# Kernel tuning notes

Hardware: AMD Instinct MI355X
Metric: run time of the kernel (lower is better)

Reference implementation:

```python
import jax, jax.numpy as jnp
import numpy as np

T, J, D = 65536, 512, 128

def setup_inputs() -> dict:
    key = jax.random.key(0)
    k1, k2 = jax.random.split(key)
    u = jax.random.normal(k1, (1, J, D), dtype=jnp.float32)
    s = jax.random.normal(k2, (T, J), dtype=jnp.float32)
    return {"u": u, "s": s}

def reference(u, s):
    # softmax over the query axis (axis=1 of s, matching tf softmax(s, axis=1))
    A = jax.nn.softmax(s, axis=1)          # [T, J]
    # sum_j A[t, j] * u[0, j, :]  == A @ u[0]
    c2q = jnp.einsum('tj,jd->td', A, u[0])  # [T, D]
    return c2q.T                            # [D, T], matching tf.transpose(c2q)
```

## Files before the change

### kernel.cpp

```cpp
#include <hip/hip_runtime.h>
#include <hip/hip_bf16.h>


constexpr int T_DIM = 65536;
constexpr int J_DIM = 512;
constexpr int D_DIM = 128;
constexpr int KK_STEPS = J_DIM / 32;
constexpr int NFRAG = 8;
constexpr int PF_DEPTH = 4;
constexpr int BP_ELEMS = KK_STEPS * NFRAG * 64;

typedef __attribute__((ext_vector_type(4))) float  f32x4;
typedef __attribute__((ext_vector_type(8))) short  s16x8;
typedef __attribute__((ext_vector_type(8))) __bf16 bf16x8;

__device__ __forceinline__ short f2bf_rne(float f) {
    unsigned u = __builtin_bit_cast(unsigned, f);
    u += 0x7fffu + ((u >> 16) & 1u);
    return (short)(u >> 16);
}

__global__ __launch_bounds__(512, 2) void c2q_main(const float* __restrict__ sm,
                                                   const float* __restrict__ u,
                                                   float* __restrict__ out) {
    __shared__ s16x8 bsh[BP_ELEMS];

    const int tid  = threadIdx.x;
    const int l    = tid & 63;
    const int w    = tid >> 6;
    const int lmod = l & 15;
    const int lh   = l >> 4;
    const int r0   = blockIdx.x * 128 + w * 16;

    const float* sp = sm + (size_t)(r0 + lmod) * J_DIM + lh * 8;

    f32x4 sbuf[PF_DEPTH][2];
#pragma unroll
    for (int p = 0; p < PF_DEPTH; ++p) {
        sbuf[p][0] = *reinterpret_cast<const f32x4*>(sp + p * 32);
        sbuf[p][1] = *reinterpret_cast<const f32x4*>(sp + p * 32 + 4);
    }

#pragma unroll 4
    for (int it = 0; it < BP_ELEMS / 512; ++it) {
        int e  = it * 512 + tid;
        int d  = ((e >> 6) & (NFRAG - 1)) * 16 + (e & 15);
        int k0 = (e >> 9) * 32 + 8 * ((e >> 4) & 3);
        const float* up = u + (size_t)k0 * D_DIM + d;
        s16x8 o;
#pragma unroll
        for (int i = 0; i < 8; ++i)
            o[i] = f2bf_rne(up[(size_t)i * D_DIM]);
        bsh[e] = o;
    }
    __syncthreads();

    f32x4 acc[NFRAG];
#pragma unroll
    for (int nf = 0; nf < NFRAG; ++nf) acc[nf] = (f32x4){0.f, 0.f, 0.f, 0.f};
    float den = 0.f;

#pragma unroll
    for (int kk = 0; kk < KK_STEPS; ++kk) {
        f32x4 s0 = sbuf[kk & (PF_DEPTH - 1)][0];
        f32x4 s1 = sbuf[kk & (PF_DEPTH - 1)][1];
        if (kk + PF_DEPTH < KK_STEPS) {
            sbuf[kk & (PF_DEPTH - 1)][0] =
                *reinterpret_cast<const f32x4*>(sp + (kk + PF_DEPTH) * 32);
            sbuf[kk & (PF_DEPTH - 1)][1] =
                *reinterpret_cast<const f32x4*>(sp + (kk + PF_DEPTH) * 32 + 4);
        }
        float e0 = __expf(s0[0]), e1 = __expf(s0[1]);
        float e2 = __expf(s0[2]), e3 = __expf(s0[3]);
        float e4 = __expf(s1[0]), e5 = __expf(s1[1]);
        float e6 = __expf(s1[2]), e7 = __expf(s1[3]);
        den += ((e0 + e1) + (e2 + e3)) + ((e4 + e5) + (e6 + e7));
        s16x8 a;
        a[0] = f2bf_rne(e0); a[1] = f2bf_rne(e1);
        a[2] = f2bf_rne(e2); a[3] = f2bf_rne(e3);
        a[4] = f2bf_rne(e4); a[5] = f2bf_rne(e5);
        a[6] = f2bf_rne(e6); a[7] = f2bf_rne(e7);
        bf16x8 av = __builtin_bit_cast(bf16x8, a);
#pragma unroll
        for (int nf = 0; nf < NFRAG; ++nf) {
            bf16x8 bv = __builtin_bit_cast(bf16x8, bsh[(kk * NFRAG + nf) * 64 + l]);
            acc[nf] = __builtin_amdgcn_mfma_f32_16x16x32_bf16(av, bv, acc[nf], 0, 0, 0);
        }
        __builtin_amdgcn_sched_barrier(0);
    }

    den += __shfl_xor(den, 16, 64);
    den += __shfl_xor(den, 32, 64);
    float inv[4];
#pragma unroll
    for (int r = 0; r < 4; ++r)
        inv[r] = 1.0f / __shfl(den, 4 * lh + r, 64);

#pragma unroll
    for (int nf = 0; nf < NFRAG; ++nf) {
        f32x4 v;
#pragma unroll
        for (int r = 0; r < 4; ++r) v[r] = acc[nf][r] * inv[r];
        *reinterpret_cast<f32x4*>(out + (size_t)(nf * 16 + lmod) * T_DIM
                                  + r0 + 4 * lh) = v;
    }
}

extern "C" void kernel_launch(void* const* d_in, const int* in_sizes, int n_in,
                              void* d_out, int out_size, void* d_ws, size_t ws_size,
                              hipStream_t stream) {
    const float* u = (const float*)d_in[0];
    const float* s = (const float*)d_in[1];
    float* out = (float*)d_out;

    c2q_main<<<T_DIM / 128, 512, 0, stream>>>(s, u, out);
}
```

Before: 38.72 us.

## Process two row tiles per block to amortize LDS B-fragment staging

Each block now handles 256 rows in two passes of 128, reusing the bf16 u fragments staged in shared memory and halving the number of blocks that convert u. The s prefetch ring is deepened to 6 and continues across the pass boundary, so loads for the second tile are issued while the first is still computing. This adds register pressure from the deeper prefetch and halves the grid to 256 blocks, which may leave fewer waves to hide latency.

Result: faster. 36.75 us (-5.1%).

```diff
diff --git a/kernel.cpp b/kernel.cpp
--- a/kernel.cpp
+++ b/kernel.cpp
@@ -7,7 +7,7 @@
 constexpr int D_DIM = 128;
 constexpr int KK_STEPS = J_DIM / 32;
 constexpr int NFRAG = 8;
-constexpr int PF_DEPTH = 4;
+constexpr int PF_DEPTH = 6;
 constexpr int BP_ELEMS = KK_STEPS * NFRAG * 64;
 
 typedef __attribute__((ext_vector_type(4))) float  f32x4;
@@ -30,15 +30,16 @@
     const int w    = tid >> 6;
     const int lmod = l & 15;
     const int lh   = l >> 4;
-    const int r0   = blockIdx.x * 128 + w * 16;
+    const int r0   = blockIdx.x * 256 + w * 16;
 
-    const float* sp = sm + (size_t)(r0 + lmod) * J_DIM + lh * 8;
+    const float* sp0 = sm + (size_t)(r0 + lmod) * J_DIM + lh * 8;
+    const float* sp1 = sp0 + 128 * J_DIM;
 
     f32x4 sbuf[PF_DEPTH][2];
 #pragma unroll
     for (int p = 0; p < PF_DEPTH; ++p) {
-        sbuf[p][0] = *reinterpret_cast<const f32x4*>(sp + p * 32);
-        sbuf[p][1] = *reinterpret_cast<const f32x4*>(sp + p * 32 + 4);
+        sbuf[p][0] = *reinterpret_cast<const f32x4*>(sp0 + p * 32);
+        sbuf[p][1] = *reinterpret_cast<const f32x4*>(sp0 + p * 32 + 4);
     }
 
 #pragma unroll 4
@@ -55,54 +56,62 @@
     }
     __syncthreads();
 
-    f32x4 acc[NFRAG];
 #pragma unroll
-    for (int nf = 0; nf < NFRAG; ++nf) acc[nf] = (f32x4){0.f, 0.f, 0.f, 0.f};
-    float den = 0.f;
+    for (int p = 0; p < 2; ++p) {
+        const int rp = r0 + p * 128;
+
+        f32x4 acc[NFRAG];
+#pragma unroll
+        for (int nf = 0; nf < NFRAG; ++nf) acc[nf] = (f32x4){0.f, 0.f, 0.f, 0.f};
+        float den = 0.f;
 
 #pragma unroll
-    for (int kk = 0; kk < KK_STEPS; ++kk) {
-        f32x4 s0 = sbuf[kk & (PF_DEPTH - 1)][0];
-        f32x4 s1 = sbuf[kk & (PF_DEPTH - 1)][1];
-        if (kk + PF_DEPTH < KK_STEPS) {
-            sbuf[kk & (PF_DEPTH - 1)][0] =
-                *reinterpret_cast<const f32x4*>(sp + (kk + PF_DEPTH) * 32);
-            sbuf[kk & (PF_DEPTH - 1)][1] =
-                *reinterpret_cast<const f32x4*>(sp + (kk + PF_DEPTH) * 32 + 4);
+        for (int kk = 0; kk < KK_STEPS; ++kk) {
+            const int g    = p * KK_STEPS + kk;
+            const int slot = g % PF_DEPTH;
+            f32x4 s0 = sbuf[slot][0];
+            f32x4 s1 = sbuf[slot][1];
+            if (g + PF_DEPTH < 2 * KK_STEPS) {
+                const int   f  = g + PF_DEPTH;
+                const float* b = (f < KK_STEPS) ? sp0 : sp1;
+                const int   tk = f & (KK_STEPS - 1);
+                sbuf[slot][0] = *reinterpret_cast<const f32x4*>(b + tk * 32);
+                sbuf[slot][1] = *reinterpret_cast<const f32x4*>(b + tk * 32 + 4);
+            }
+            float e0 = __expf(s0[0]), e1 = __expf(s0[1]);
+            float e2 = __expf(s0[2]), e3 = __expf(s0[3]);
+            float e4 = __expf(s1[0]), e5 = __expf(s1[1]);
+            float e6 = __expf(s1[2]), e7 = __expf(s1[3]);
+            den += ((e0 + e1) + (e2 + e3)) + ((e4 + e5) + (e6 + e7));
+            s16x8 a;
+            a[0] = f2bf_rne(e0); a[1] = f2bf_rne(e1);
+            a[2] = f2bf_rne(e2); a[3] = f2bf_rne(e3);
+            a[4] = f2bf_rne(e4); a[5] = f2bf_rne(e5);
+            a[6] = f2bf_rne(e6); a[7] = f2bf_rne(e7);
+            bf16x8 av = __builtin_bit_cast(bf16x8, a);
+#pragma unroll
+            for (int nf = 0; nf < NFRAG; ++nf) {
+                bf16x8 bv = __builtin_bit_cast(bf16x8, bsh[(kk * NFRAG + nf) * 64 + l]);
+                acc[nf] = __builtin_amdgcn_mfma_f32_16x16x32_bf16(av, bv, acc[nf], 0, 0, 0);
+            }
+            __builtin_amdgcn_sched_barrier(0);
         }
-        float e0 = __expf(s0[0]), e1 = __expf(s0[1]);
-        float e2 = __expf(s0[2]), e3 = __expf(s0[3]);
-        float e4 = __expf(s1[0]), e5 = __expf(s1[1]);
-        float e6 = __expf(s1[2]), e7 = __expf(s1[3]);
-        den += ((e0 + e1) + (e2 + e3)) + ((e4 + e5) + (e6 + e7));
-        s16x8 a;
-        a[0] = f2bf_rne(e0); a[1] = f2bf_rne(e1);
-        a[2] = f2bf_rne(e2); a[3] = f2bf_rne(e3);
-        a[4] = f2bf_rne(e4); a[5] = f2bf_rne(e5);
-        a[6] = f2bf_rne(e6); a[7] = f2bf_rne(e7);
-        bf16x8 av = __builtin_bit_cast(bf16x8, a);
+
+        den += __shfl_xor(den, 16, 64);
+        den += __shfl_xor(den, 32, 64);
+        float inv[4];
+#pragma unroll
+        for (int r = 0; r < 4; ++r)
+            inv[r] = 1.0f / __shfl(den, 4 * lh + r, 64);
+
 #pragma unroll
         for (int nf = 0; nf < NFRAG; ++nf) {
-            bf16x8 bv = __builtin_bit_cast(bf16x8, bsh[(kk * NFRAG + nf) * 64 + l]);
-            acc[nf] = __builtin_amdgcn_mfma_f32_16x16x32_bf16(av, bv, acc[nf], 0, 0, 0);
+            f32x4 v;
+#pragma unroll
+            for (int r = 0; r < 4; ++r) v[r] = acc[nf][r] * inv[r];
+            *reinterpret_cast<f32x4*>(out + (size_t)(nf * 16 + lmod) * T_DIM
+                                      + rp + 4 * lh) = v;
         }
-        __builtin_amdgcn_sched_barrier(0);
-    }
-
-    den += __shfl_xor(den, 16, 64);
-    den += __shfl_xor(den, 32, 64);
-    float inv[4];
-#pragma unroll
-    for (int r = 0; r < 4; ++r)
-        inv[r] = 1.0f / __shfl(den, 4 * lh + r, 64);
-
-#pragma unroll
-    for (int nf = 0; nf < NFRAG; ++nf) {
-        f32x4 v;
-#pragma unroll
-        for (int r = 0; r < 4; ++r) v[r] = acc[nf][r] * inv[r];
-        *reinterpret_cast<f32x4*>(out + (size_t)(nf * 16 + lmod) * T_DIM
-                                  + r0 + 4 * lh) = v;
     }
 }
 
@@ -113,5 +122,5 @@
     const float* s = (const float*)d_in[1];
     float* out = (float*)d_out;
 
-    c2q_main<<<T_DIM / 128, 512, 0, stream>>>(s, u, out);
+    c2q_main<<<T_DIM / 256, 512, 0, stream>>>(s, u, out);
 }
```

## Split bf16 B staging into two half-size LDS passes to cut shared memory

Applied to the files above, without the earlier changes.

The converted u operand is now staged in LDS in two halves (first 256 rows, then the remaining 256) instead of all 512 rows at once, which halves the shared-memory footprint per block. The likely aim is to fit more blocks per CU, or ease LDS pressure, so more s-row streaming is in flight. In exchange it adds two block-wide barriers and a second fill partway through the K loop, which stalls all waves while the second half is converted from global memory.

After: 42.28 us. 9.2% more time.

```diff
diff --git a/kernel.cpp b/kernel.cpp
--- a/kernel.cpp
+++ b/kernel.cpp
@@ -5,10 +5,11 @@
 constexpr int T_DIM = 65536;
 constexpr int J_DIM = 512;
 constexpr int D_DIM = 128;
-constexpr int KK_STEPS = J_DIM / 32;
+constexpr int KK_PER_PASS = 8;
+constexpr int NSTEP = 16;
 constexpr int NFRAG = 8;
 constexpr int PF_DEPTH = 4;
-constexpr int BP_ELEMS = KK_STEPS * NFRAG * 64;
+constexpr int BP_ELEMS = KK_PER_PASS * NFRAG * 64;
 
 typedef __attribute__((ext_vector_type(4))) float  f32x4;
 typedef __attribute__((ext_vector_type(8))) short  s16x8;
@@ -18,6 +19,22 @@
     unsigned u = __builtin_bit_cast(unsigned, f);
     u += 0x7fffu + ((u >> 16) & 1u);
     return (short)(u >> 16);
+}
+
+__device__ __forceinline__ void fill_b(int pass, const float* __restrict__ u,
+                                       s16x8* __restrict__ bsh, int tid) {
+#pragma unroll 4
+    for (int it = 0; it < BP_ELEMS / 512; ++it) {
+        int e  = it * 512 + tid;
+        int d  = ((e >> 6) & (NFRAG - 1)) * 16 + (e & 15);
+        int k0 = pass * 256 + (e >> 9) * 32 + 8 * ((e >> 4) & 3);
+        const float* up = u + (size_t)k0 * D_DIM + d;
+        s16x8 o;
+#pragma unroll
+        for (int i = 0; i < 8; ++i)
+            o[i] = f2bf_rne(up[(size_t)i * D_DIM]);
+        bsh[e] = o;
+    }
 }
 
 __global__ __launch_bounds__(512, 2) void c2q_main(const float* __restrict__ sm,
@@ -41,18 +58,7 @@
         sbuf[p][1] = *reinterpret_cast<const f32x4*>(sp + p * 32 + 4);
     }
 
-#pragma unroll 4
-    for (int it = 0; it < BP_ELEMS / 512; ++it) {
-        int e  = it * 512 + tid;
-        int d  = ((e >> 6) & (NFRAG - 1)) * 16 + (e & 15);
-        int k0 = (e >> 9) * 32 + 8 * ((e >> 4) & 3);
-        const float* up = u + (size_t)k0 * D_DIM + d;
-        s16x8 o;
-#pragma unroll
-        for (int i = 0; i < 8; ++i)
-            o[i] = f2bf_rne(up[(size_t)i * D_DIM]);
-        bsh[e] = o;
-    }
+    fill_b(0, u, bsh, tid);
     __syncthreads();
 
     f32x4 acc[NFRAG];
@@ -61,14 +67,20 @@
     float den = 0.f;
 
 #pragma unroll
-    for (int kk = 0; kk < KK_STEPS; ++kk) {
-        f32x4 s0 = sbuf[kk & (PF_DEPTH - 1)][0];
-        f32x4 s1 = sbuf[kk & (PF_DEPTH - 1)][1];
-        if (kk + PF_DEPTH < KK_STEPS) {
-            sbuf[kk & (PF_DEPTH - 1)][0] =
-                *reinterpret_cast<const f32x4*>(sp + (kk + PF_DEPTH) * 32);
-            sbuf[kk & (PF_DEPTH - 1)][1] =
-                *reinterpret_cast<const f32x4*>(sp + (kk + PF_DEPTH) * 32 + 4);
+    for (int g = 0; g < NSTEP; ++g) {
+        if (g == KK_PER_PASS) {
+            __syncthreads();
+            fill_b(1, u, bsh, tid);
+            __syncthreads();
+        }
+        const int slot = g & (PF_DEPTH - 1);
+        f32x4 s0 = sbuf[slot][0];
+        f32x4 s1 = sbuf[slot][1];
+        if (g + PF_DEPTH < NSTEP) {
+            sbuf[slot][0] =
+                *reinterpret_cast<const f32x4*>(sp + (g + PF_DEPTH) * 32);
+            sbuf[slot][1] =
+                *reinterpret_cast<const f32x4*>(sp + (g + PF_DEPTH) * 32 + 4);
         }
         float e0 = __expf(s0[0]), e1 = __expf(s0[1]);
         float e2 = __expf(s0[2]), e3 = __expf(s0[3]);
@@ -81,6 +93,7 @@
         a[4] = f2bf_rne(e4); a[5] = f2bf_rne(e5);
         a[6] = f2bf_rne(e6); a[7] = f2bf_rne(e7);
         bf16x8 av = __builtin_bit_cast(bf16x8, a);
+        const int kk = g & (KK_PER_PASS - 1);
 #pragma unroll
         for (int nf = 0; nf < NFRAG; ++nf) {
             bf16x8 bv = __builtin_bit_cast(bf16x8, bsh[(kk * NFRAG + nf) * 64 + l]);
```

## Switch to 32x32x16 MFMA tiles with 32 rows per wave

Applied to the files above, without the earlier changes.

Replaces the 16x16x32 bf16 MFMA with 32x32x16, so each wave handles 32 rows of s and each block handles 256. Each iteration loads and exponentiates twice as many s values per lane, and the B operand layout in LDS is repacked to match. This aims to cut LDS reads and MFMA instruction overhead per output. The cost is that the grid shrinks to half as many blocks, which lowers parallelism across CUs, and the accumulators use more registers.

New measurement: 51.14 us. +32.1%, slower.

```diff
diff --git a/kernel.cpp b/kernel.cpp
--- a/kernel.cpp
+++ b/kernel.cpp
@@ -5,14 +5,15 @@
 constexpr int T_DIM = 65536;
 constexpr int J_DIM = 512;
 constexpr int D_DIM = 128;
-constexpr int KK_STEPS = J_DIM / 32;
-constexpr int NFRAG = 8;
+constexpr int KK = 16;
+constexpr int NFRAG = 4;
 constexpr int PF_DEPTH = 4;
-constexpr int BP_ELEMS = KK_STEPS * NFRAG * 64;
+constexpr int BP_ELEMS = KK * 2 * NFRAG * 64;
 
-typedef __attribute__((ext_vector_type(4))) float  f32x4;
-typedef __attribute__((ext_vector_type(8))) short  s16x8;
-typedef __attribute__((ext_vector_type(8))) __bf16 bf16x8;
+typedef __attribute__((ext_vector_type(4)))  float  f32x4;
+typedef __attribute__((ext_vector_type(16))) float  f32x16;
+typedef __attribute__((ext_vector_type(8)))  short  s16x8;
+typedef __attribute__((ext_vector_type(8)))  __bf16 bf16x8;
 
 __device__ __forceinline__ short f2bf_rne(float f) {
     unsigned u = __builtin_bit_cast(unsigned, f);
@@ -28,24 +29,26 @@
     const int tid  = threadIdx.x;
     const int l    = tid & 63;
     const int w    = tid >> 6;
-    const int lmod = l & 15;
-    const int lh   = l >> 4;
-    const int r0   = blockIdx.x * 128 + w * 16;
+    const int l31  = l & 31;
+    const int lh5  = l >> 5;
+    const int r0w  = blockIdx.x * 256 + w * 32;
 
-    const float* sp = sm + (size_t)(r0 + lmod) * J_DIM + lh * 8;
+    const float* sp = sm + (size_t)(r0w + l31) * J_DIM + lh5 * 8;
 
-    f32x4 sbuf[PF_DEPTH][2];
+    f32x4 sbuf[PF_DEPTH][4];
 #pragma unroll
     for (int p = 0; p < PF_DEPTH; ++p) {
         sbuf[p][0] = *reinterpret_cast<const f32x4*>(sp + p * 32);
         sbuf[p][1] = *reinterpret_cast<const f32x4*>(sp + p * 32 + 4);
+        sbuf[p][2] = *reinterpret_cast<const f32x4*>(sp + p * 32 + 16);
+        sbuf[p][3] = *reinterpret_cast<const f32x4*>(sp + p * 32 + 20);
     }
 
 #pragma unroll 4
     for (int it = 0; it < BP_ELEMS / 512; ++it) {
         int e  = it * 512 + tid;
-        int d  = ((e >> 6) & (NFRAG - 1)) * 16 + (e & 15);
-        int k0 = (e >> 9) * 32 + 8 * ((e >> 4) & 3);
+        int d  = ((e >> 6) & 3) * 32 + (e & 31);
+        int k0 = (e >> 9) * 32 + ((e >> 8) & 1) * 16 + ((e >> 5) & 1) * 8;
         const float* up = u + (size_t)k0 * D_DIM + d;
         s16x8 o;
 #pragma unroll
@@ -55,54 +58,80 @@
     }
     __syncthreads();
 
-    f32x4 acc[NFRAG];
+    f32x16 acc[NFRAG];
 #pragma unroll
-    for (int nf = 0; nf < NFRAG; ++nf) acc[nf] = (f32x4){0.f, 0.f, 0.f, 0.f};
+    for (int nf = 0; nf < NFRAG; ++nf)
+#pragma unroll
+        for (int r = 0; r < 16; ++r) acc[nf][r] = 0.f;
     float den = 0.f;
 
 #pragma unroll
-    for (int kk = 0; kk < KK_STEPS; ++kk) {
-        f32x4 s0 = sbuf[kk & (PF_DEPTH - 1)][0];
-        f32x4 s1 = sbuf[kk & (PF_DEPTH - 1)][1];
-        if (kk + PF_DEPTH < KK_STEPS) {
-            sbuf[kk & (PF_DEPTH - 1)][0] =
-                *reinterpret_cast<const f32x4*>(sp + (kk + PF_DEPTH) * 32);
-            sbuf[kk & (PF_DEPTH - 1)][1] =
-                *reinterpret_cast<const f32x4*>(sp + (kk + PF_DEPTH) * 32 + 4);
+    for (int g = 0; g < KK; ++g) {
+        const int slot = g & (PF_DEPTH - 1);
+        f32x4 s0 = sbuf[slot][0];
+        f32x4 s1 = sbuf[slot][1];
+        f32x4 s2 = sbuf[slot][2];
+        f32x4 s3 = sbuf[slot][3];
+        if (g + PF_DEPTH < KK) {
+            const float* b = sp + (g + PF_DEPTH) * 32;
+            sbuf[slot][0] = *reinterpret_cast<const f32x4*>(b);
+            sbuf[slot][1] = *reinterpret_cast<const f32x4*>(b + 4);
+            sbuf[slot][2] = *reinterpret_cast<const f32x4*>(b + 16);
+            sbuf[slot][3] = *reinterpret_cast<const f32x4*>(b + 20);
         }
         float e0 = __expf(s0[0]), e1 = __expf(s0[1]);
         float e2 = __expf(s0[2]), e3 = __expf(s0[3]);
         float e4 = __expf(s1[0]), e5 = __expf(s1[1]);
         float e6 = __expf(s1[2]), e7 = __expf(s1[3]);
-        den += ((e0 + e1) + (e2 + e3)) + ((e4 + e5) + (e6 + e7));
-        s16x8 a;
-        a[0] = f2bf_rne(e0); a[1] = f2bf_rne(e1);
-        a[2] = f2bf_rne(e2); a[3] = f2bf_rne(e3);
-        a[4] = f2bf_rne(e4); a[5] = f2bf_rne(e5);
-        a[6] = f2bf_rne(e6); a[7] = f2bf_rne(e7);
-        bf16x8 av = __builtin_bit_cast(bf16x8, a);
+        float f0 = __expf(s2[0]), f1 = __expf(s2[1]);
+        float f2 = __expf(s2[2]), f3 = __expf(s2[3]);
+        float f4 = __expf(s3[0]), f5 = __expf(s3[1]);
+        float f6 = __expf(s3[2]), f7 = __expf(s3[3]);
+        den += ((e0 + e1) + (e2 + e3)) + ((e4 + e5) + (e6 + e7))
+             + ((f0 + f1) + (f2 + f3)) + ((f4 + f5) + (f6 + f7));
+        s16x8 a0, a1;
+        a0[0] = f2bf_rne(e0); a0[1] = f2bf_rne(e1);
+        a0[2] = f2bf_rne(e2); a0[3] = f2bf_rne(e3);
+        a0[4] = f2bf_rne(e4); a0[5] = f2bf_rne(e5);
+        a0[6] = f2bf_rne(e6); a0[7] = f2bf_rne(e7);
+        a1[0] = f2bf_rne(f0); a1[1] = f2bf_rne(f1);
+        a1[2] = f2bf_rne(f2); a1[3] = f2bf_rne(f3);
+        a1[4] = f2bf_rne(f4); a1[5] = f2bf_rne(f5);
+        a1[6] = f2bf_rne(f6); a1[7] = f2bf_rne(f7);
+        bf16x8 av0 = __builtin_bit_cast(bf16x8, a0);
+        bf16x8 av1 = __builtin_bit_cast(bf16x8, a1);
 #pragma unroll
         for (int nf = 0; nf < NFRAG; ++nf) {
-            bf16x8 bv = __builtin_bit_cast(bf16x8, bsh[(kk * NFRAG + nf) * 64 + l]);
-            acc[nf] = __builtin_amdgcn_mfma_f32_16x16x32_bf16(av, bv, acc[nf], 0, 0, 0);
+            bf16x8 b0 = __builtin_bit_cast(bf16x8,
+                bsh[((g * 2 + 0) * NFRAG + nf) * 64 + l]);
+            acc[nf] = __builtin_amdgcn_mfma_f32_32x32x16_bf16(av0, b0, acc[nf], 0, 0, 0);
+            bf16x8 b1 = __builtin_bit_cast(bf16x8,
+                bsh[((g * 2 + 1) * NFRAG + nf) * 64 + l]);
+            acc[nf] = __builtin_amdgcn_mfma_f32_32x32x16_bf16(av1, b1, acc[nf], 0, 0, 0);
         }
         __builtin_amdgcn_sched_barrier(0);
     }
 
-    den += __shfl_xor(den, 16, 64);
     den += __shfl_xor(den, 32, 64);
-    float inv[4];
+    float inv[4][4];
 #pragma unroll
-    for (int r = 0; r < 4; ++r)
-        inv[r] = 1.0f / __shfl(den, 4 * lh + r, 64);
+    for (int q = 0; q < 4; ++q) {
+        const int rbase = 8 * q + 4 * lh5;
+#pragma unroll
+        for (int j = 0; j < 4; ++j)
+            inv[q][j] = 1.0f / __shfl(den, rbase + j, 64);
+    }
 
 #pragma unroll
     for (int nf = 0; nf < NFRAG; ++nf) {
-        f32x4 v;
 #pragma unroll
-        for (int r = 0; r < 4; ++r) v[r] = acc[nf][r] * inv[r];
-        *reinterpret_cast<f32x4*>(out + (size_t)(nf * 16 + lmod) * T_DIM
-                                  + r0 + 4 * lh) = v;
+        for (int q = 0; q < 4; ++q) {
+            f32x4 v;
+#pragma unroll
+            for (int j = 0; j < 4; ++j) v[j] = acc[nf][4 * q + j] * inv[q][j];
+            *reinterpret_cast<f32x4*>(out + (size_t)(nf * 32 + l31) * T_DIM
+                                      + r0w + 8 * q + 4 * lh5) = v;
+        }
     }
 }
 
@@ -113,5 +142,5 @@
     const float* s = (const float*)d_in[1];
     float* out = (float*)d_out;
 
-    c2q_main<<<T_DIM / 128, 512, 0, stream>>>(s, u, out);
+    c2q_main<<<T_DIM / 256, 512, 0, stream>>>(s, u, out);
 }
```
